# Optimization experiments

Measured on AMD Instinct MI355X. Metric: run time of the kernel, lower is better.

Reference implementation:

```python
import jax, jax.numpy as jnp
import numpy as np

NUM_CHUNKS = 8
TOP_K = 2
IN_F = 4096
HID_F = 4096
OUT_F = 4096
B = 4096


def setup_inputs() -> dict:
    key = jax.random.key(0)
    k = jax.random.split(key, 5)
    cin = IN_F // NUM_CHUNKS    # 512
    cout = HID_F // NUM_CHUNKS  # 512
    s_in = 1.0 / np.sqrt(cin)
    s_fin = 1.0 / np.sqrt(cout * TOP_K)
    return {
        "x": jax.random.normal(k[0], (B, IN_F), dtype=jnp.float32),
        # stacked chunk-expert Linear params: y = x @ W + b
        "W_chunks": jax.random.uniform(k[1], (NUM_CHUNKS, cin, cout), jnp.float32, -s_in, s_in),
        "b_chunks": jax.random.uniform(k[2], (NUM_CHUNKS, cout), jnp.float32, -s_in, s_in),
        "W_final": jax.random.uniform(k[3], (cout * TOP_K, OUT_F), jnp.float32, -s_fin, s_fin),
        "b_final": jax.random.uniform(k[4], (OUT_F,), jnp.float32, -s_fin, s_fin),
    }


def reference(x, W_chunks, b_chunks, W_final, b_final):
    Bsz = x.shape[0]
    # split into chunks along feature dim: (B, num_chunks, chunk_in)
    xr = x.reshape(Bsz, NUM_CHUNKS, -1)
    # per-chunk activity = mean(|chunk|) over the whole batch (matches torch .abs().mean())
    activities = jnp.mean(jnp.abs(xr), axis=(0, 2))  # (num_chunks,)
    _, topk_idx = jax.lax.top_k(activities, TOP_K)    # descending, like torch.topk
    # gather selected chunks and their expert weights, run small GEMMs
    x_sel = xr[:, topk_idx, :]                        # (B, k, chunk_in)
    h = jnp.einsum('bkc,kcd->bkd', x_sel, W_chunks[topk_idx]) + b_chunks[topk_idx]
    h = h.reshape(Bsz, -1)                            # concat along feature dim
    out = h @ W_final + b_final                       # (B, out_features)
    return out
```

## Files before the change

### kernel.cpp

```cpp
#include <hip/hip_runtime.h>
#include <type_traits>


typedef __bf16 bf16x8_t __attribute__((ext_vector_type(8)));
typedef float  f32x4_t  __attribute__((ext_vector_type(4)));

__device__ inline unsigned short f2bf(float f) {
    __bf16 b = (__bf16)f;
    return __builtin_bit_cast(unsigned short, b);
}

__global__ void activity_kernel(const float* __restrict__ x, float* __restrict__ act) {
    const int chunk = blockIdx.y;
    const int tid = threadIdx.x;
    const int colf4 = tid & 127;
    const int rsub = tid >> 7;
    const float4* base = (const float4*)x + (size_t)chunk * 128 + colf4;
    float s = 0.f;
    #pragma unroll 4
    for (int i = 0; i < 32; ++i) {
        int row = blockIdx.x * 64 + i * 2 + rsub;
        float4 v = base[(size_t)row * 1024];
        s += fabsf(v.x) + fabsf(v.y) + fabsf(v.z) + fabsf(v.w);
    }
    #pragma unroll
    for (int off = 32; off > 0; off >>= 1) s += __shfl_down(s, off, 64);
    __shared__ float wsum[4];
    if ((tid & 63) == 0) wsum[tid >> 6] = s;
    __syncthreads();
    if (tid == 0) atomicAdd(&act[chunk], wsum[0] + wsum[1] + wsum[2] + wsum[3]);
}

__global__ void topk_kernel(const float* __restrict__ act, int* __restrict__ idx) {
    if (threadIdx.x == 0) {
        float v0 = -1e30f, v1 = -1e30f; int b0 = 0, b1 = 0;
        for (int i = 0; i < 8; ++i) {
            float v = act[i];
            if (v > v0) { v1 = v0; b1 = b0; v0 = v; b0 = i; }
            else if (v > v1) { v1 = v; b1 = i; }
        }
        idx[0] = b0; idx[1] = b1;
    }
}

__global__ void gather_x_kernel(const float* __restrict__ x, const int* __restrict__ idx,
                                unsigned short* __restrict__ xb) {
    int t = blockIdx.x * blockDim.x + threadIdx.x;
    int row = t >> 8;
    int c4 = (t & 255) * 4;
    int kk = c4 >> 9;
    int scol = idx[kk] * 512 + (c4 & 511);
    float4 v = *(const float4*)(x + (size_t)row * 4096 + scol);
    ushort4 o;
    o.x = f2bf(v.x); o.y = f2bf(v.y); o.z = f2bf(v.z); o.w = f2bf(v.w);
    *(ushort4*)(xb + (size_t)row * 1024 + c4) = o;
}

__global__ void transpose_cvt_kernel(const float* __restrict__ src, unsigned short* __restrict__ dst,
                                     int R, int C, const int* __restrict__ idx, int chunk_elems) {
    if (idx) { src += (size_t)idx[blockIdx.z] * chunk_elems; dst += (size_t)blockIdx.z * chunk_elems; }
    __shared__ float tile[32][33];
    const int tx = threadIdx.x, ty = threadIdx.y;
    const int cb = blockIdx.x * 32, rb = blockIdx.y * 32;
    #pragma unroll
    for (int i = 0; i < 4; ++i)
        tile[ty + i * 8][tx] = src[(size_t)(rb + ty + i * 8) * C + cb + tx];
    __syncthreads();
    #pragma unroll
    for (int i = 0; i < 4; ++i)
        dst[(size_t)(cb + ty + i * 8) * R + rb + tx] = f2bf(tile[tx][ty + i * 8]);
}

#define BM 128
#define BN 128
#define BKT 64
#define LDT 72

template <typename OutT>
__global__ __launch_bounds__(256, 2)
void gemm_bt_kernel(const unsigned short* __restrict__ A, int lda, int aOffZ,
                    const unsigned short* __restrict__ Bt, int ldb, int bOffZ,
                    OutT* __restrict__ C, int ldc, int cOffZ,
                    const float* __restrict__ biasBase, int biasStride,
                    const int* __restrict__ idxPtr, int K) {
    const int z = blockIdx.z;
    A  += (size_t)z * aOffZ;
    Bt += (size_t)z * bOffZ;
    C  += (size_t)z * cOffZ;
    const float* bias = biasBase + (idxPtr ? (size_t)idxPtr[z] * biasStride : 0);

    __shared__ unsigned short As[BM * LDT];
    __shared__ unsigned short Bs[BN * LDT];

    const int tid = threadIdx.x;
    const int wave = tid >> 6;
    const int lane = tid & 63;
    const int m0 = blockIdx.x * BM;
    const int n0 = blockIdx.y * BN;
    const int wm = (wave >> 1) * 64;
    const int wn = (wave & 1) * 64;

    f32x4_t acc[4][4] = {};

    const int sr = tid >> 3;
    const int sc = (tid & 7) * 8;

    for (int k0 = 0; k0 < K; k0 += BKT) {
        #pragma unroll
        for (int p = 0; p < 4; ++p) {
            int r = p * 32 + sr;
            uint4 va = *(const uint4*)(A  + (size_t)(m0 + r) * lda + k0 + sc);
            uint4 vb = *(const uint4*)(Bt + (size_t)(n0 + r) * ldb + k0 + sc);
            *(uint4*)(As + r * LDT + sc) = va;
            *(uint4*)(Bs + r * LDT + sc) = vb;
        }
        __syncthreads();
        #pragma unroll
        for (int kq = 0; kq < 2; ++kq) {
            const int kb = kq * 32 + ((lane >> 4) * 8);
            bf16x8_t af[4], bfr[4];
            #pragma unroll
            for (int i = 0; i < 4; ++i) {
                af[i]  = *(const bf16x8_t*)(As + (wm + i * 16 + (lane & 15)) * LDT + kb);
                bfr[i] = *(const bf16x8_t*)(Bs + (wn + i * 16 + (lane & 15)) * LDT + kb);
            }
            #pragma unroll
            for (int mi = 0; mi < 4; ++mi)
                #pragma unroll
                for (int ni = 0; ni < 4; ++ni)
                    acc[mi][ni] = __builtin_amdgcn_mfma_f32_16x16x32_bf16(af[mi], bfr[ni], acc[mi][ni], 0, 0, 0);
        }
        __syncthreads();
    }

    const int row_l = (lane >> 4) * 4;
    const int col_l = lane & 15;
    #pragma unroll
    for (int mi = 0; mi < 4; ++mi) {
        #pragma unroll
        for (int ni = 0; ni < 4; ++ni) {
            int col = n0 + wn + ni * 16 + col_l;
            float bv = bias[col];
            #pragma unroll
            for (int j = 0; j < 4; ++j) {
                int row = m0 + wm + mi * 16 + row_l + j;
                float v = acc[mi][ni][j] + bv;
                if constexpr (std::is_same<OutT, unsigned short>::value)
                    C[(size_t)row * ldc + col] = f2bf(v);
                else
                    C[(size_t)row * ldc + col] = v;
            }
        }
    }
}

extern "C" void kernel_launch(void* const* d_in, const int* in_sizes, int n_in,
                              void* d_out, int out_size, void* d_ws, size_t ws_size,
                              hipStream_t stream) {
    const float* x    = (const float*)d_in[0];
    const float* Wc   = (const float*)d_in[1];
    const float* bc   = (const float*)d_in[2];
    const float* Wf   = (const float*)d_in[3];
    const float* bfin = (const float*)d_in[4];
    float* out = (float*)d_out;

    float* act = (float*)d_ws;
    int*   idx = (int*)((char*)d_ws + 64);
    unsigned short* xb  = (unsigned short*)((char*)d_ws + 256);
    unsigned short* h   = xb  + (size_t)4096 * 1024;
    unsigned short* wct = h   + (size_t)4096 * 1024;
    unsigned short* wft = wct + (size_t)2 * 512 * 512;

    hipMemsetAsync(d_ws, 0, 64, stream);

    activity_kernel<<<dim3(64, 8), 256, 0, stream>>>(x, act);
    topk_kernel<<<1, 64, 0, stream>>>(act, idx);
    gather_x_kernel<<<4096, 256, 0, stream>>>(x, idx, xb);
    transpose_cvt_kernel<<<dim3(16, 16, 2), dim3(32, 8), 0, stream>>>(Wc, wct, 512, 512, idx, 512 * 512);
    transpose_cvt_kernel<<<dim3(128, 32, 1), dim3(32, 8), 0, stream>>>(Wf, wft, 1024, 4096, nullptr, 0);

    gemm_bt_kernel<unsigned short><<<dim3(32, 4, 2), 256, 0, stream>>>(
        xb, 1024, 512, wct, 512, 512 * 512, h, 1024, 512, bc, 512, idx, 512);

    gemm_bt_kernel<float><<<dim3(32, 32, 1), 256, 0, stream>>>(
        h, 1024, 0, wft, 1024, 0, out, 4096, 0, bfin, 0, nullptr, 1024);
}
```

Baseline: 215.4 us.

## Fuse gather/convert into GEMM1, use direct-to-LDS loads with XOR swizzle

The separate gather-and-convert kernel goes away. GEMM1 now reads the selected fp32 chunk of x directly, converts it to bf16 and writes it into a swizzled shared-memory tile, which saves one round trip of the gathered activations through memory. GEMM2 and the weight side of GEMM1 stage tiles with global_load_lds and an XOR swizzle instead of a padded layout, which cuts register traffic and LDS bank conflicts. The atomic-plus-memset activity reduction is replaced by per-block partials that the top-k kernel reduces, and GEMM1 moves to 64x64 tiles for more blocks.

```diff
diff --git a/kernel.cpp b/kernel.cpp
--- a/kernel.cpp
+++ b/kernel.cpp
@@ -1,5 +1,4 @@
 #include <hip/hip_runtime.h>
-#include <type_traits>
 
 
 typedef __bf16 bf16x8_t __attribute__((ext_vector_type(8)));
@@ -10,7 +9,23 @@
     return __builtin_bit_cast(unsigned short, b);
 }
 
-__global__ void activity_kernel(const float* __restrict__ x, float* __restrict__ act) {
+
+__device__ inline void stage_glds(const unsigned short* gtile, int stride, int row0,
+                                  unsigned short* lds, int lane) {
+    const int r8 = lane >> 3;
+    const int gg = (lane & 7) ^ r8;
+    const unsigned short* gp = gtile + (size_t)(row0 + r8) * stride + gg * 8;
+    unsigned short* lp = lds + row0 * 64;
+    __builtin_amdgcn_global_load_lds((const __attribute__((address_space(1))) void*)gp,
+                                     (__attribute__((address_space(3))) void*)lp,
+                                     16, 0, 0);
+}
+
+__device__ inline bf16x8_t ldsfrag(const unsigned short* Ls, int row, int kb) {
+    return *(const bf16x8_t*)(Ls + row * 64 + (((kb >> 3) ^ (row & 7)) * 8));
+}
+
+__global__ void activity_kernel(const float* __restrict__ x, float* __restrict__ part) {
     const int chunk = blockIdx.y;
     const int tid = threadIdx.x;
     const int colf4 = tid & 127;
@@ -28,10 +43,18 @@
     __shared__ float wsum[4];
     if ((tid & 63) == 0) wsum[tid >> 6] = s;
     __syncthreads();
-    if (tid == 0) atomicAdd(&act[chunk], wsum[0] + wsum[1] + wsum[2] + wsum[3]);
-}
-
-__global__ void topk_kernel(const float* __restrict__ act, int* __restrict__ idx) {
+    if (tid == 0) part[chunk * 64 + blockIdx.x] = wsum[0] + wsum[1] + wsum[2] + wsum[3];
+}
+
+__global__ void topk_kernel(const float* __restrict__ part, int* __restrict__ idx) {
+    __shared__ float act[8];
+    const int lane = threadIdx.x & 63;
+    const int wave = threadIdx.x >> 6;
+    float s = part[wave * 64 + lane];
+    #pragma unroll
+    for (int off = 32; off > 0; off >>= 1) s += __shfl_down(s, off, 64);
+    if (lane == 0) act[wave] = s;
+    __syncthreads();
     if (threadIdx.x == 0) {
         float v0 = -1e30f, v1 = -1e30f; int b0 = 0, b1 = 0;
         for (int i = 0; i < 8; ++i) {
@@ -43,19 +66,6 @@
     }
 }
 
-__global__ void gather_x_kernel(const float* __restrict__ x, const int* __restrict__ idx,
-                                unsigned short* __restrict__ xb) {
-    int t = blockIdx.x * blockDim.x + threadIdx.x;
-    int row = t >> 8;
-    int c4 = (t & 255) * 4;
-    int kk = c4 >> 9;
-    int scol = idx[kk] * 512 + (c4 & 511);
-    float4 v = *(const float4*)(x + (size_t)row * 4096 + scol);
-    ushort4 o;
-    o.x = f2bf(v.x); o.y = f2bf(v.y); o.z = f2bf(v.z); o.w = f2bf(v.w);
-    *(ushort4*)(xb + (size_t)row * 1024 + c4) = o;
-}
-
 __global__ void transpose_cvt_kernel(const float* __restrict__ src, unsigned short* __restrict__ dst,
                                      int R, int C, const int* __restrict__ idx, int chunk_elems) {
     if (idx) { src += (size_t)idx[blockIdx.z] * chunk_elems; dst += (size_t)blockIdx.z * chunk_elems; }
@@ -71,58 +81,122 @@
         dst[(size_t)(cb + ty + i * 8) * R + rb + tx] = f2bf(tile[tx][ty + i * 8]);
 }
 
-#define BM 128
-#define BN 128
-#define BKT 64
-#define LDT 72
-
-template <typename OutT>
 __global__ __launch_bounds__(256, 2)
-void gemm_bt_kernel(const unsigned short* __restrict__ A, int lda, int aOffZ,
-                    const unsigned short* __restrict__ Bt, int ldb, int bOffZ,
-                    OutT* __restrict__ C, int ldc, int cOffZ,
-                    const float* __restrict__ biasBase, int biasStride,
-                    const int* __restrict__ idxPtr, int K) {
+void gemm1_kernel(const float* __restrict__ x, const unsigned short* __restrict__ wct,
+                  const float* __restrict__ bc, const int* __restrict__ idx,
+                  unsigned short* __restrict__ h) {
     const int z = blockIdx.z;
-    A  += (size_t)z * aOffZ;
-    Bt += (size_t)z * bOffZ;
-    C  += (size_t)z * cOffZ;
-    const float* bias = biasBase + (idxPtr ? (size_t)idxPtr[z] * biasStride : 0);
-
-    __shared__ unsigned short As[BM * LDT];
-    __shared__ unsigned short Bs[BN * LDT];
+    const int idxz = idx[z];
+    const int m0 = blockIdx.x * 64;
+    const int n0 = blockIdx.y * 64;
+
+    __shared__ unsigned short As[64 * 64];
+    __shared__ unsigned short Bs[64 * 64];
 
     const int tid = threadIdx.x;
     const int wave = tid >> 6;
     const int lane = tid & 63;
-    const int m0 = blockIdx.x * BM;
-    const int n0 = blockIdx.y * BN;
+    const int wm = (wave >> 1) * 32;
+    const int wn = (wave & 1) * 32;
+    const int rl = lane & 15;
+    const int quad = lane >> 4;
+
+    const float* xtile = x + (size_t)m0 * 4096 + idxz * 512;
+    const unsigned short* bttile = wct + (size_t)z * 512 * 512 + (size_t)n0 * 512;
+
+    f32x4_t acc[2][2] = {};
+
+    const int ar = tid >> 2;
+    const int aq = tid & 3;
+
+    for (int k0 = 0; k0 < 512; k0 += 64) {
+        #pragma unroll
+        for (int s = wave; s < 8; s += 4)
+            stage_glds(bttile + k0, 512, s * 8, Bs, lane);
+        const float* gr = xtile + (size_t)ar * 4096 + k0;
+        #pragma unroll
+        for (int j = 0; j < 2; ++j) {
+            int gg = aq * 2 + j;
+            float4 a = *(const float4*)(gr + gg * 8);
+            float4 b = *(const float4*)(gr + gg * 8 + 4);
+            bf16x8_t v;
+            v[0] = (__bf16)a.x; v[1] = (__bf16)a.y; v[2] = (__bf16)a.z; v[3] = (__bf16)a.w;
+            v[4] = (__bf16)b.x; v[5] = (__bf16)b.y; v[6] = (__bf16)b.z; v[7] = (__bf16)b.w;
+            *(bf16x8_t*)(As + ar * 64 + ((gg ^ (ar & 7)) * 8)) = v;
+        }
+        __syncthreads();
+        #pragma unroll
+        for (int kq = 0; kq < 2; ++kq) {
+            const int kb = kq * 32 + quad * 8;
+            bf16x8_t af[2], bfr[2];
+            #pragma unroll
+            for (int i = 0; i < 2; ++i) {
+                af[i]  = ldsfrag(As, wm + i * 16 + rl, kb);
+                bfr[i] = ldsfrag(Bs, wn + i * 16 + rl, kb);
+            }
+            #pragma unroll
+            for (int mi = 0; mi < 2; ++mi)
+                #pragma unroll
+                for (int ni = 0; ni < 2; ++ni)
+                    acc[mi][ni] = __builtin_amdgcn_mfma_f32_16x16x32_bf16(af[mi], bfr[ni], acc[mi][ni], 0, 0, 0);
+        }
+        __syncthreads();
+    }
+
+    const int row_l = quad * 4;
+    const float* bias = bc + (size_t)idxz * 512;
+    #pragma unroll
+    for (int ni = 0; ni < 2; ++ni) {
+        int col = n0 + wn + ni * 16 + rl;
+        float bv = bias[col];
+        #pragma unroll
+        for (int mi = 0; mi < 2; ++mi) {
+            #pragma unroll
+            for (int j = 0; j < 4; ++j) {
+                int row = m0 + wm + mi * 16 + row_l + j;
+                h[(size_t)row * 1024 + z * 512 + col] = f2bf(acc[mi][ni][j] + bv);
+            }
+        }
+    }
+}
+
+__global__ __launch_bounds__(256, 2)
+void gemm2_kernel(const unsigned short* __restrict__ A, const unsigned short* __restrict__ Bt,
+                  const float* __restrict__ bias, float* __restrict__ C) {
+    const int m0 = blockIdx.x * 128;
+    const int n0 = blockIdx.y * 128;
+
+    __shared__ unsigned short As[128 * 64];
+    __shared__ unsigned short Bs[128 * 64];
+
+    const int tid = threadIdx.x;
+    const int wave = tid >> 6;
+    const int lane = tid & 63;
     const int wm = (wave >> 1) * 64;
     const int wn = (wave & 1) * 64;
+    const int rl = lane & 15;
+    const int quad = lane >> 4;
+
+    const unsigned short* Atile = A + (size_t)m0 * 1024;
+    const unsigned short* Btile = Bt + (size_t)n0 * 1024;
 
     f32x4_t acc[4][4] = {};
 
-    const int sr = tid >> 3;
-    const int sc = (tid & 7) * 8;
-
-    for (int k0 = 0; k0 < K; k0 += BKT) {
-        #pragma unroll
-        for (int p = 0; p < 4; ++p) {
-            int r = p * 32 + sr;
-            uint4 va = *(const uint4*)(A  + (size_t)(m0 + r) * lda + k0 + sc);
-            uint4 vb = *(const uint4*)(Bt + (size_t)(n0 + r) * ldb + k0 + sc);
-            *(uint4*)(As + r * LDT + sc) = va;
-            *(uint4*)(Bs + r * LDT + sc) = vb;
+    for (int k0 = 0; k0 < 1024; k0 += 64) {
+        #pragma unroll
+        for (int s = wave; s < 32; s += 4) {
+            if (s < 16) stage_glds(Atile + k0, 1024, s * 8, As, lane);
+            else        stage_glds(Btile + k0, 1024, (s - 16) * 8, Bs, lane);
         }
         __syncthreads();
         #pragma unroll
         for (int kq = 0; kq < 2; ++kq) {
-            const int kb = kq * 32 + ((lane >> 4) * 8);
+            const int kb = kq * 32 + quad * 8;
             bf16x8_t af[4], bfr[4];
             #pragma unroll
             for (int i = 0; i < 4; ++i) {
-                af[i]  = *(const bf16x8_t*)(As + (wm + i * 16 + (lane & 15)) * LDT + kb);
-                bfr[i] = *(const bf16x8_t*)(Bs + (wn + i * 16 + (lane & 15)) * LDT + kb);
+                af[i]  = ldsfrag(As, wm + i * 16 + rl, kb);
+                bfr[i] = ldsfrag(Bs, wn + i * 16 + rl, kb);
             }
             #pragma unroll
             for (int mi = 0; mi < 4; ++mi)
@@ -133,22 +207,19 @@
         __syncthreads();
     }
 
-    const int row_l = (lane >> 4) * 4;
-    const int col_l = lane & 15;
+    const int row_l = quad * 4;
+    float bv[4];
+    #pragma unroll
+    for (int ni = 0; ni < 4; ++ni) bv[ni] = bias[n0 + wn + ni * 16 + rl];
     #pragma unroll
     for (int mi = 0; mi < 4; ++mi) {
         #pragma unroll
         for (int ni = 0; ni < 4; ++ni) {
-            int col = n0 + wn + ni * 16 + col_l;
-            float bv = bias[col];
+            int col = n0 + wn + ni * 16 + rl;
             #pragma unroll
             for (int j = 0; j < 4; ++j) {
                 int row = m0 + wm + mi * 16 + row_l + j;
-                float v = acc[mi][ni][j] + bv;
-                if constexpr (std::is_same<OutT, unsigned short>::value)
-                    C[(size_t)row * ldc + col] = f2bf(v);
-                else
-                    C[(size_t)row * ldc + col] = v;
+                C[(size_t)row * 4096 + col] = acc[mi][ni][j] + bv[ni];
             }
         }
     }
@@ -164,24 +235,17 @@
     const float* bfin = (const float*)d_in[4];
     float* out = (float*)d_out;
 
-    float* act = (float*)d_ws;
-    int*   idx = (int*)((char*)d_ws + 64);
-    unsigned short* xb  = (unsigned short*)((char*)d_ws + 256);
-    unsigned short* h   = xb  + (size_t)4096 * 1024;
+    float* part = (float*)d_ws;
+    int*   idx  = (int*)((char*)d_ws + 2048);
+    unsigned short* h   = (unsigned short*)((char*)d_ws + 4096);
     unsigned short* wct = h   + (size_t)4096 * 1024;
     unsigned short* wft = wct + (size_t)2 * 512 * 512;
 
-    hipMemsetAsync(d_ws, 0, 64, stream);
-
-    activity_kernel<<<dim3(64, 8), 256, 0, stream>>>(x, act);
-    topk_kernel<<<1, 64, 0, stream>>>(act, idx);
-    gather_x_kernel<<<4096, 256, 0, stream>>>(x, idx, xb);
+    activity_kernel<<<dim3(64, 8), 256, 0, stream>>>(x, part);
+    topk_kernel<<<1, 512, 0, stream>>>(part, idx);
     transpose_cvt_kernel<<<dim3(16, 16, 2), dim3(32, 8), 0, stream>>>(Wc, wct, 512, 512, idx, 512 * 512);
     transpose_cvt_kernel<<<dim3(128, 32, 1), dim3(32, 8), 0, stream>>>(Wf, wft, 1024, 4096, nullptr, 0);
 
-    gemm_bt_kernel<unsigned short><<<dim3(32, 4, 2), 256, 0, stream>>>(
-        xb, 1024, 512, wct, 512, 512 * 512, h, 1024, 512, bc, 512, idx, 512);
-
-    gemm_bt_kernel<float><<<dim3(32, 32, 1), 256, 0, stream>>>(
-        h, 1024, 0, wft, 1024, 0, out, 4096, 0, bfin, 0, nullptr, 1024);
-}
+    gemm1_kernel<<<dim3(64, 8, 2), 256, 0, stream>>>(x, wct, bc, idx, h);
+    gemm2_kernel<<<dim3(32, 32, 1), 256, 0, stream>>>(h, wft, bfin, out);
+}
```

After: 193.1 us. 1.12x faster.
